# Kernel optimization log

Measured on AMD Instinct MI355X. Metric: run time of the kernel, lower is better.

Reference implementation:

```python
import jax, jax.numpy as jnp
import numpy as np

EPS = 1e-7  # K.epsilon()
ATTN_WIDTH = 12
B, L, D = 8, 4096, 768


def setup_inputs() -> dict:
    key = jax.random.key(0)
    k1, k2 = jax.random.split(key)
    x = jax.random.normal(k1, (B, L, D), dtype=jnp.float32)
    Wa = jax.random.normal(k2, (D, 1), dtype=jnp.float32) * 0.05  # RandomNormal(stddev=0.05)
    return {"x": x, "Wa": Wa}


def reference(x, Wa):
    """Banded rank-1 self-attention.

    e[b,i,j] = u[b,i]*u[b,j] with u = x @ Wa, masked to the trailing band
    i-w+1 <= j <= i, normalized by the row sum (+eps), then v = a @ x.
    Because e is rank-1 inside the band, we never materialize the LxL matrix:
      wsum_i  = sum_{j=i-w+1}^{i} u_j          (windowed cumsum)
      wvec_i  = sum_{j=i-w+1}^{i} u_j * x_j    (windowed cumsum of u*x)
      v_i     = u_i * wvec_i / (u_i * wsum_i + eps)
    which is exactly e/(sum(e)+eps) @ x.
    """
    w = ATTN_WIDTH
    u = jnp.einsum('bld,do->bl', x, Wa)            # [B, L]
    cu = jnp.cumsum(u, axis=1)                      # [B, L]
    cux = jnp.cumsum(u[..., None] * x, axis=1)      # [B, L, D]
    # shifted[i] = cu[i-w] (0 for i < w)
    cu_shift = jnp.pad(cu, ((0, 0), (w, 0)))[:, :L]
    cux_shift = jnp.pad(cux, ((0, 0), (w, 0), (0, 0)))[:, :L, :]
    wsum = cu - cu_shift                            # [B, L]
    wvec = cux - cux_shift                          # [B, L, D]
    denom = u * wsum + EPS                          # [B, L]
    v = (u[..., None] * wvec) / denom[..., None]    # [B, L, D]
    return v
```

## Files before the change

kernel.cpp:

```cpp
#include <hip/hip_runtime.h>

typedef float vfloat4 __attribute__((ext_vector_type(4)));

namespace {
constexpr int kB = 8;
constexpr int kL = 4096;
constexpr int kD = 768;
constexpr int kW = 12;
constexpr int kHalo = kW - 1;
constexpr float kEps = 1e-7f;

constexpr int kRowsPerBlockU = 16;
constexpr int kGridU = kB * kL / kRowsPerBlockU;

constexpr int kT2 = 8;
constexpr int kRing = kT2 + kHalo;
constexpr int kThreads2 = 192;
constexpr int kChunks2 = kL / kT2;
constexpr int kGridV = kB * kChunks2;
}

__global__ __launch_bounds__(256, 4) void compute_u_kernel(
    const float* __restrict__ x, const float* __restrict__ Wa,
    double* __restrict__ u) {
  const int lane = threadIdx.x & 63;
  const int wv = threadIdx.x >> 6;
  const int rg0 = blockIdx.x * kRowsPerBlockU + wv * 4;

  vfloat4 w[3];
#pragma unroll
  for (int k = 0; k < 3; ++k)
    w[k] = *(const vfloat4*)(Wa + 4 * lane + 256 * k);

  vfloat4 xv[4][3];
#pragma unroll
  for (int q = 0; q < 4; ++q)
#pragma unroll
    for (int k = 0; k < 3; ++k)
      xv[q][k] = *(const vfloat4*)(x + (size_t)(rg0 + q) * kD + 4 * lane + 256 * k);

  double acc[4];
#pragma unroll
  for (int q = 0; q < 4; ++q) {
    double p = 0.0;
#pragma unroll
    for (int k = 0; k < 3; ++k) {
      p += (double)xv[q][k].x * (double)w[k].x + (double)xv[q][k].y * (double)w[k].y +
           (double)xv[q][k].z * (double)w[k].z + (double)xv[q][k].w * (double)w[k].w;
    }
    acc[q] = p;
  }
#pragma unroll
  for (int q = 0; q < 4; ++q) {
#pragma unroll
    for (int s = 32; s >= 1; s >>= 1) acc[q] += __shfl_xor(acc[q], s, 64);
  }
  if (lane == 0) {
#pragma unroll
    for (int q = 0; q < 4; ++q) u[rg0 + q] = acc[q];
  }
}

__global__ __launch_bounds__(kThreads2, 3) void banded_v_kernel(
    const float* __restrict__ x, const double* __restrict__ u,
    float* __restrict__ out) {
  const int blk = blockIdx.x;
  const int b = blk / kChunks2;
  const int i0 = (blk % kChunks2) * kT2;
  const float* xb = x + (size_t)b * kL * kD;
  float* ob = out + (size_t)b * kL * kD;
  const double* ub = u + (size_t)b * kL;
  const int tid = threadIdx.x;
  const int lane = tid & 63;
  const int c0 = 4 * tid;

  vfloat4 xr[kRing];
  float ufr[kRing];
  if (i0 >= kHalo) {
#pragma unroll
    for (int r = 0; r < kRing; ++r)
      xr[r] = *(const vfloat4*)(xb + (size_t)(i0 - kHalo + r) * kD + c0);
#pragma unroll
    for (int r = 0; r < kRing; ++r)
      ufr[r] = (float)ub[i0 - kHalo + r];
  } else {
#pragma unroll
    for (int r = 0; r < kRing; ++r) {
      const int row = i0 - kHalo + r;
      vfloat4 v = {0.f, 0.f, 0.f, 0.f};
      float uu = 0.0f;
      if (row >= 0) {
        v = *(const vfloat4*)(xb + (size_t)row * kD + c0);
        uu = (float)ub[row];
      }
      xr[r] = v;
      ufr[r] = uu;
    }
  }

  {
    const int myt = lane & 7;
    const int il = i0 + myt;
    double wsum = 0.0;
#pragma unroll
    for (int k = 0; k < kW; ++k) {
      const int j = il - kHalo + k;
      if (j >= 0) wsum += ub[j];
    }
    const double uu = ub[il];
    const float msc = (float)(uu / (uu * wsum + (double)kEps));
    float sc[kT2];
#pragma unroll
    for (int t = 0; t < kT2; ++t) sc[t] = __shfl(msc, t, 8);

#pragma unroll
    for (int t = 0; t < kT2; ++t) {
      vfloat4 acc = {0.f, 0.f, 0.f, 0.f};
#pragma unroll
      for (int j = 0; j < kW; ++j) {
        const int r = kHalo + t - j;
        const float uu2 = ufr[r];
        const vfloat4 xv = xr[r];
        acc.x += uu2 * xv.x; acc.y += uu2 * xv.y;
        acc.z += uu2 * xv.z; acc.w += uu2 * xv.w;
      }
      const float s = sc[t];
      vfloat4 o = {s * acc.x, s * acc.y, s * acc.z, s * acc.w};
      __builtin_nontemporal_store(o, (vfloat4*)(ob + (size_t)(i0 + t) * kD + c0));
    }
  }
}

extern "C" void kernel_launch(void* const* d_in, const int* in_sizes, int n_in,
                              void* d_out, int out_size, void* d_ws, size_t ws_size,
                              hipStream_t stream) {
  const float* x = (const float*)d_in[0];
  const float* Wa = (const float*)d_in[1];
  float* out = (float*)d_out;
  double* u = (double*)d_ws;
  (void)ws_size;

  compute_u_kernel<<<kGridU, 256, 0, stream>>>(x, Wa, u);
  banded_v_kernel<<<kGridV, kThreads2, 0, stream>>>(x, u, out);
}
```

Measured before the change: 213.7 us.

## Stream 32-row strips per wave with register ring buffer and running window sum

Measured after the change: 195.0 us. 8.8% less time.

```diff
diff --git a/kernel.cpp b/kernel.cpp
--- a/kernel.cpp
+++ b/kernel.cpp
@@ -13,11 +13,14 @@
 constexpr int kRowsPerBlockU = 16;
 constexpr int kGridU = kB * kL / kRowsPerBlockU;
 
-constexpr int kT2 = 8;
-constexpr int kRing = kT2 + kHalo;
-constexpr int kThreads2 = 192;
-constexpr int kChunks2 = kL / kT2;
-constexpr int kGridV = kB * kChunks2;
+constexpr int kS = 32;
+constexpr int kSlots = 16;
+constexpr int kSMask = kSlots - 1;
+constexpr int kThirds = 3;
+constexpr int kStripsPerB = kL / kS;
+constexpr int kWavesK2 = kB * kStripsPerB * kThirds;
+constexpr int kThreads2 = 256;
+constexpr int kGrid2 = kWavesK2 * 64 / kThreads2;
 }
 
 __global__ __launch_bounds__(256, 4) void compute_u_kernel(
@@ -61,72 +64,81 @@
   }
 }
 
-__global__ __launch_bounds__(kThreads2, 3) void banded_v_kernel(
+__global__ __launch_bounds__(kThreads2, 3) void banded_stencil_kernel(
     const float* __restrict__ x, const double* __restrict__ u,
     float* __restrict__ out) {
-  const int blk = blockIdx.x;
-  const int b = blk / kChunks2;
-  const int i0 = (blk % kChunks2) * kT2;
-  const float* xb = x + (size_t)b * kL * kD;
-  float* ob = out + (size_t)b * kL * kD;
-  const double* ub = u + (size_t)b * kL;
-  const int tid = threadIdx.x;
-  const int lane = tid & 63;
-  const int c0 = 4 * tid;
+  const int wid = (int)((blockIdx.x * kThreads2 + threadIdx.x) >> 6);
+  const int lane = threadIdx.x & 63;
+  const int b = wid / (kStripsPerB * kThirds);
+  const int rem = wid % (kStripsPerB * kThirds);
+  const int s = rem / kThirds;
+  const int h = rem % kThirds;
+  const int i0 = s * kS;
+  const float* xb = x + (size_t)b * kL * kD + 256 * h + 4 * lane;
+  float* ob = out + (size_t)b * kL * kD + 256 * h + 4 * lane;
+  const double* ubase = u + (size_t)b * kL;
 
-  vfloat4 xr[kRing];
-  float ufr[kRing];
+  vfloat4 xr[kSlots];
+  double ud[kSlots];
+  float uf[kSlots];
+
   if (i0 >= kHalo) {
 #pragma unroll
-    for (int r = 0; r < kRing; ++r)
-      xr[r] = *(const vfloat4*)(xb + (size_t)(i0 - kHalo + r) * kD + c0);
+    for (int r = 0; r < kSlots; ++r)
+      xr[r] = *(const vfloat4*)(xb + (size_t)(i0 - kHalo + r) * kD);
 #pragma unroll
-    for (int r = 0; r < kRing; ++r)
-      ufr[r] = (float)ub[i0 - kHalo + r];
+    for (int r = 0; r < kSlots; ++r) {
+      const double du = ubase[i0 - kHalo + r];
+      ud[r] = du;
+      uf[r] = (float)du;
+    }
   } else {
 #pragma unroll
-    for (int r = 0; r < kRing; ++r) {
+    for (int r = 0; r < kSlots; ++r) {
       const int row = i0 - kHalo + r;
       vfloat4 v = {0.f, 0.f, 0.f, 0.f};
-      float uu = 0.0f;
+      double du = 0.0;
       if (row >= 0) {
-        v = *(const vfloat4*)(xb + (size_t)row * kD + c0);
-        uu = (float)ub[row];
+        v = *(const vfloat4*)(xb + (size_t)row * kD);
+        du = ubase[row];
       }
       xr[r] = v;
-      ufr[r] = uu;
+      ud[r] = du;
+      uf[r] = (float)du;
     }
   }
 
-  {
-    const int myt = lane & 7;
-    const int il = i0 + myt;
-    double wsum = 0.0;
+  double wsum_p = 0.0;
 #pragma unroll
-    for (int k = 0; k < kW; ++k) {
-      const int j = il - kHalo + k;
-      if (j >= 0) wsum += ub[j];
-    }
-    const double uu = ub[il];
-    const float msc = (float)(uu / (uu * wsum + (double)kEps));
-    float sc[kT2];
-#pragma unroll
-    for (int t = 0; t < kT2; ++t) sc[t] = __shfl(msc, t, 8);
+  for (int r = 0; r < kHalo; ++r) wsum_p += ud[r];
 
 #pragma unroll
-    for (int t = 0; t < kT2; ++t) {
-      vfloat4 acc = {0.f, 0.f, 0.f, 0.f};
+  for (int t = 0; t < kS; ++t) {
+    const int r = kHalo + t;
+    const double uu = ud[r & kSMask];
+    const double wsum = wsum_p + uu;
+    const float sc = (float)(uu / (uu * wsum + (double)kEps));
+
+    vfloat4 acc = {0.f, 0.f, 0.f, 0.f};
 #pragma unroll
-      for (int j = 0; j < kW; ++j) {
-        const int r = kHalo + t - j;
-        const float uu2 = ufr[r];
-        const vfloat4 xv = xr[r];
-        acc.x += uu2 * xv.x; acc.y += uu2 * xv.y;
-        acc.z += uu2 * xv.z; acc.w += uu2 * xv.w;
-      }
-      const float s = sc[t];
-      vfloat4 o = {s * acc.x, s * acc.y, s * acc.z, s * acc.w};
-      __builtin_nontemporal_store(o, (vfloat4*)(ob + (size_t)(i0 + t) * kD + c0));
+    for (int j = 0; j < kW; ++j) {
+      const int rs = (r - j) & kSMask;
+      const float w = uf[rs];
+      const vfloat4 xv = xr[rs];
+      acc.x += w * xv.x; acc.y += w * xv.y;
+      acc.z += w * xv.z; acc.w += w * xv.w;
+    }
+    vfloat4 o = {sc * acc.x, sc * acc.y, sc * acc.z, sc * acc.w};
+    __builtin_nontemporal_store(o, (vfloat4*)(ob + (size_t)(i0 + t) * kD));
+
+    wsum_p = wsum - ud[(r - kHalo) & kSMask];
+
+    if (t + kSlots <= kS + kHalo - 1) {
+      const int row = i0 - kHalo + t + kSlots;
+      xr[t & kSMask] = *(const vfloat4*)(xb + (size_t)row * kD);
+      const double nu = ubase[row];
+      ud[t & kSMask] = nu;
+      uf[t & kSMask] = (float)nu;
     }
   }
 }
@@ -141,5 +153,5 @@
   (void)ws_size;
 
   compute_u_kernel<<<kGridU, 256, 0, stream>>>(x, Wa, u);
-  banded_v_kernel<<<kGridV, kThreads2, 0, stream>>>(x, u, out);
+  banded_stencil_kernel<<<kGrid2, kThreads2, 0, stream>>>(x, u, out);
 }
```
